# Kernel optimization log

Hardware: AMD Instinct MI355X
Metric: run time of the kernel (lower is better)

Reference implementation:

```python
import jax, jax.numpy as jnp
import numpy as np

B, S, D = 4, 2048, 1024
H, E = 16, 64  # n_heads, head_size; H*E == D


def setup_inputs() -> dict:
    key = jax.random.key(0)
    ks = jax.random.split(key, 6)
    sd = 1.0 / np.sqrt(D)
    x = jax.random.normal(ks[0], (B, S, D), dtype=jnp.float32)
    # per-head Q/K/V projection weights, stacked: [H, D, E]
    Wq = jax.random.uniform(ks[1], (H, D, E), jnp.float32, -sd, sd)
    Wk = jax.random.uniform(ks[2], (H, D, E), jnp.float32, -sd, sd)
    Wv = jax.random.uniform(ks[3], (H, D, E), jnp.float32, -sd, sd)
    Wp = jax.random.uniform(ks[4], (D, D), jnp.float32, -sd, sd)
    bp = jax.random.uniform(ks[5], (D,), jnp.float32, -sd, sd)
    return {"x": x, "Wq": Wq, "Wk": Wk, "Wv": Wv, "Wp": Wp, "bp": bp}


def reference(x, Wq, Wk, Wv, Wp, bp):
    # Per-head projections (all heads batched): [B, H, S, E]
    q = jnp.einsum('bsd,hde->bhse', x, Wq)
    k = jnp.einsum('bsd,hde->bhse', x, Wk)
    v = jnp.einsum('bsd,hde->bhse', x, Wv)
    scale = E ** -0.5
    # Full causal score matrix [B, H, S, S]
    wei = jnp.einsum('bhse,bhte->bhst', q, k) * scale
    causal = jnp.tril(jnp.ones((S, S), dtype=bool))
    wei = jnp.where(causal, wei, -jnp.inf)
    wei = jax.nn.softmax(wei, axis=-1)
    out = jnp.einsum('bhst,bhte->bhse', wei, v)
    # concat heads along feature dim: [B, S, H*E]
    out = out.transpose(0, 2, 1, 3).reshape(B, S, H * E)
    # output projection (dropout is identity in eval)
    return out @ Wp.T + bp
```

## Files before the change

kernel.cpp:

```cpp
#include <hip/hip_runtime.h>

#define B_ 4
#define S_ 2048
#define D_ 1024
#define H_ 16
#define E_ 64
#define M_ (B_*S_)

typedef __attribute__((ext_vector_type(8))) short short8;
typedef __attribute__((ext_vector_type(4))) float floatx4;

#define GLD16(g, l) __builtin_amdgcn_global_load_lds( \
    (const __attribute__((address_space(1))) unsigned*)(g), \
    (__attribute__((address_space(3))) unsigned*)(l), 16, 0, 0)

__device__ __forceinline__ ushort f2b(float f) {
    union { float f; unsigned u; } v; v.f = f;
    unsigned r = v.u + 0x7fffu + ((v.u >> 16) & 1u);
    return (ushort)(r >> 16);
}
__device__ __forceinline__ unsigned cvt_pk_bf16(float lo, float hi) {
    unsigned r;
    asm("v_cvt_pk_bf16_f32 %0, %1, %2" : "=v"(r) : "v"(lo), "v"(hi));
    return r;
}
__device__ __forceinline__ float fast_exp2(float x) {
#if __has_builtin(__builtin_amdgcn_exp2f)
    return __builtin_amdgcn_exp2f(x);
#else
    float r; asm("v_exp_f32 %0, %1" : "=v"(r) : "v"(x)); return r;
#endif
}
__device__ __forceinline__ float lane_pull(float v, int srclane) {
    return __int_as_float(__builtin_amdgcn_ds_bpermute(srclane << 2, __float_as_int(v)));
}

__global__ __launch_bounds__(256) void prologue(const float* __restrict__ x,
                                                const float* __restrict__ Wq,
                                                const float* __restrict__ Wk,
                                                const float* __restrict__ Wv,
                                                const float* __restrict__ Wp,
                                                ushort* __restrict__ xb,
                                                ushort* __restrict__ wpb,
                                                ushort* __restrict__ wt) {
    __shared__ __align__(16) ushort T[64 * 80];
    const int bid = blockIdx.x;
    const int t = threadIdx.x;

    if (bid < 2048) {
        const int n8 = (int)((size_t)M_ * D_ / 8);
        int i = bid * 256 + t;
        const int stride = 2048 * 256;
        for (; i < n8; i += stride) {
            float4 a = ((const float4*)x)[2 * i];
            float4 b = ((const float4*)x)[2 * i + 1];
            short8 o;
            o[0] = (short)f2b(a.x); o[1] = (short)f2b(a.y);
            o[2] = (short)f2b(a.z); o[3] = (short)f2b(a.w);
            o[4] = (short)f2b(b.x); o[5] = (short)f2b(b.y);
            o[6] = (short)f2b(b.z); o[7] = (short)f2b(b.w);
            ((short8*)xb)[i] = o;
        }
    } else if (bid < 2560) {
        int i = (bid - 2048) * 256 + t;
        float4 a = ((const float4*)Wp)[2 * i];
        float4 b = ((const float4*)Wp)[2 * i + 1];
        short8 o;
        o[0] = (short)f2b(a.x); o[1] = (short)f2b(a.y);
        o[2] = (short)f2b(a.z); o[3] = (short)f2b(a.w);
        o[4] = (short)f2b(b.x); o[5] = (short)f2b(b.y);
        o[6] = (short)f2b(b.z); o[7] = (short)f2b(b.w);
        ((short8*)wpb)[i] = o;
    } else {
        const int q = bid - 2560;
        const int g = q >> 4;
        const int d0 = (q & 15) * 64;
        const float* W = (g < 16 ? Wq : (g < 32 ? Wk : Wv)) + (size_t)(g & 15) * (D_ * E_);
        #pragma unroll
        for (int it = 0; it < 4; ++it) {
            int i = it * 256 + t;
            int r = i >> 4, c = i & 15;
            float4 xx = *(const float4*)(W + (size_t)(d0 + r) * E_ + c * 4);
            T[(c * 4 + 0) * 80 + r] = f2b(xx.x);
            T[(c * 4 + 1) * 80 + r] = f2b(xx.y);
            T[(c * 4 + 2) * 80 + r] = f2b(xx.z);
            T[(c * 4 + 3) * 80 + r] = f2b(xx.w);
        }
        __syncthreads();
        #pragma unroll
        for (int it = 0; it < 2; ++it) {
            int i = it * 256 + t;
            int e = i >> 3, c = i & 7;
            short8 xx = *(const short8*)&T[e * 80 + c * 8];
            *(short8*)&wt[((size_t)g * E_ + e) * D_ + d0 + c * 8] = xx;
        }
    }
}

__global__ __launch_bounds__(512) void gemm_qkv(const ushort* __restrict__ xb,
                                                const ushort* __restrict__ wt,
                                                ushort* __restrict__ qk,
                                                ushort* __restrict__ vt) {
    const int m0 = blockIdx.x * 256;
    const int n0 = blockIdx.y * 128;
    const int w  = n0 >> 10;

    __shared__ __align__(16) ushort As[2][256 * 32];
    __shared__ __align__(16) ushort Bs[2][128 * 32];

    const int t = threadIdx.x, l = t & 63, wid = t >> 6;
    const int wm = (wid & 3) * 64, wn = (wid >> 2) * 64;
    floatx4 acc[4][4] = {};

    {
        #pragma unroll
        for (int it = 0; it < 2; ++it) {
            int i = it * 512 + t;
            int r = i >> 2, cs = i & 3;
            int c = cs ^ ((r >> 1) & 3);
            GLD16(xb + (size_t)(m0 + r) * D_ + c * 8, &As[0][i * 8]);
        }
        int r = t >> 2, cs = t & 3;
        int c = cs ^ ((r >> 1) & 3);
        GLD16(wt + (size_t)(n0 + r) * D_ + c * 8, &Bs[0][t * 8]);
    }
    __syncthreads();

    int buf = 0;
    for (int k0 = 0; k0 < D_; k0 += 32) {
        if (k0 + 32 < D_) {
            #pragma unroll
            for (int it = 0; it < 2; ++it) {
                int i = it * 512 + t;
                int r = i >> 2, cs = i & 3;
                int c = cs ^ ((r >> 1) & 3);
                GLD16(xb + (size_t)(m0 + r) * D_ + k0 + 32 + c * 8, &As[buf ^ 1][i * 8]);
            }
            int r = t >> 2, cs = t & 3;
            int c = cs ^ ((r >> 1) & 3);
            GLD16(wt + (size_t)(n0 + r) * D_ + k0 + 32 + c * 8, &Bs[buf ^ 1][t * 8]);
        }

        short8 af[4], bf[4];
        #pragma unroll
        for (int mf = 0; mf < 4; ++mf) {
            int row = wm + 16 * mf + (l & 15);
            int c = (l >> 4) ^ ((row >> 1) & 3);
            af[mf] = *(const short8*)&As[buf][row * 32 + c * 8];
        }
        #pragma unroll
        for (int nf = 0; nf < 4; ++nf) {
            int row = wn + 16 * nf + (l & 15);
            int c = (l >> 4) ^ ((row >> 1) & 3);
            bf[nf] = *(const short8*)&Bs[buf][row * 32 + c * 8];
        }
        #pragma unroll
        for (int mf = 0; mf < 4; ++mf)
            #pragma unroll
            for (int nf = 0; nf < 4; ++nf)
                acc[mf][nf] = __builtin_amdgcn_mfma_f32_16x16x32_bf16(af[mf], bf[nf], acc[mf][nf], 0, 0, 0);

        __syncthreads();
        buf ^= 1;
    }

    if (w < 2) {
        ushort* outw = qk + (size_t)w * ((size_t)B_ * H_ * S_ * E_);
        #pragma unroll
        for (int mf = 0; mf < 4; ++mf)
            #pragma unroll
            for (int nf = 0; nf < 4; ++nf) {
                int n = n0 + wn + 16 * nf + (l & 15);
                int h = (n >> 6) & 15, e = n & 63;
                #pragma unroll
                for (int r = 0; r < 4; ++r) {
                    int m = m0 + wm + 16 * mf + (l >> 4) * 4 + r;
                    int b = m >> 11, s = m & (S_ - 1);
                    outw[((size_t)((b << 4) + h) * S_ + s) * E_ + e] = f2b(acc[mf][nf][r]);
                }
            }
    } else {
        #pragma unroll
        for (int mf = 0; mf < 4; ++mf) {
            int m = m0 + wm + 16 * mf + (l >> 4) * 4;
            int b = m >> 11, s = m & (S_ - 1);
            #pragma unroll
            for (int nf = 0; nf < 4; ++nf) {
                int n = n0 + wn + 16 * nf + (l & 15);
                int h = (n >> 6) & 15, e = n & 63;
                unsigned pk0 = cvt_pk_bf16(acc[mf][nf][0], acc[mf][nf][1]);
                unsigned pk1 = cvt_pk_bf16(acc[mf][nf][2], acc[mf][nf][3]);
                *(uint2*)&vt[((size_t)((b << 4) + h) * E_ + e) * S_ + s] = make_uint2(pk0, pk1);
            }
        }
    }
}

__global__ __launch_bounds__(256) void flash(const ushort* __restrict__ qg,
                                             const ushort* __restrict__ kg,
                                             const ushort* __restrict__ vtg,
                                             ushort* __restrict__ attn) {
    const int n = blockIdx.x;
    const int x = n >> 6;
    const int bh = n & 63;
    const int b = bh >> 4, h = bh & 15;
    const ushort* qb = qg + (size_t)bh * (S_ * E_);
    const ushort* kb = kg + (size_t)bh * (S_ * E_);
    const ushort* vb = vtg + (size_t)bh * (E_ * S_);

    __shared__ __align__(16) ushort QP[64 * 64];
    __shared__ __align__(16) ushort Ks[2][64 * 64];
    __shared__ __align__(16) ushort Vs[2][64 * 64];

    const int t = threadIdx.x, l = t & 63, wid = t >> 6;
    const float SC = 0.18033688f;
    const float NEG_INF = -__builtin_inff();
    const int g = l >> 4;
    const int qloc = l & 15;
    const int qts[2] = {x, 31 - x};
    ushort* Pw = &QP[wid * 1024];

    #pragma unroll 1
    for (int qi = 0; qi < 2; ++qi) {
        const int qt = qts[qi];

        #pragma unroll
        for (int it = 0; it < 2; ++it) {
            int i = it * 256 + t;
            int r = i >> 3, cs = i & 7, c = cs ^ (r & 7);
            GLD16(qb + (size_t)(qt * 64 + r) * E_ + c * 8, &QP[i * 8]);
            GLD16(kb + (size_t)r * E_ + c * 8, &Ks[0][i * 8]);
            GLD16(vb + (size_t)r * S_ + c * 8, &Vs[0][i * 8]);
        }
        __syncthreads();

        short8 qf[2];
        #pragma unroll
        for (int ks = 0; ks < 2; ++ks) {
            int row = wid * 16 + qloc;
            int c = (g + 4 * ks) ^ (row & 7);
            qf[ks] = *(const short8*)&QP[row * 64 + c * 8];
        }

        floatx4 o[4] = {};
        float mr = NEG_INF, lr = 0.f;

        int buf = 0;
        for (int jt = 0; jt <= qt; ++jt) {
            if (jt < qt) {
                #pragma unroll
                for (int it = 0; it < 2; ++it) {
                    int i = it * 256 + t;
                    int r = i >> 3, cs = i & 7, c = cs ^ (r & 7);
                    GLD16(kb + (size_t)((jt + 1) * 64 + r) * E_ + c * 8, &Ks[buf ^ 1][i * 8]);
                    GLD16(vb + (size_t)r * S_ + (jt + 1) * 64 + c * 8, &Vs[buf ^ 1][i * 8]);
                }
            }

            floatx4 s[4] = {};
            #pragma unroll
            for (int nf = 0; nf < 4; ++nf) {
                #pragma unroll
                for (int ks = 0; ks < 2; ++ks) {
                    int row = 16 * nf + qloc;
                    int c = (g + 4 * ks) ^ (row & 7);
                    short8 kf = *(const short8*)&Ks[buf][row * 64 + c * 8];
                    s[nf] = __builtin_amdgcn_mfma_f32_16x16x32_bf16(kf, qf[ks], s[nf], 0, 0, 0);
                }
            }

            if (jt == qt) {
                int qrow = wid * 16 + qloc;
                #pragma unroll
                for (int nf = 0; nf < 4; ++nf)
                    #pragma unroll
                    for (int r = 0; r < 4; ++r)
                        if (16 * nf + 4 * g + r > qrow) s[nf][r] = NEG_INF;
            }

            float mx = s[0][0];
            #pragma unroll
            for (int nf = 0; nf < 4; ++nf)
                #pragma unroll
                for (int r = 0; r < 4; ++r) mx = fmaxf(mx, s[nf][r]);
            mx = fmaxf(mx, __shfl_xor(mx, 16));
            mx = fmaxf(mx, __shfl_xor(mx, 32));
            bool ok = (mx - mr) * SC <= 8.0f;

            if (!__all(ok)) {
                float mn = fmaxf(mr, mx);
                float al = fast_exp2((mr - mn) * SC);
                mr = mn;
                lr *= al;
                #pragma unroll
                for (int r = 0; r < 4; ++r) {
                    float alq = lane_pull(al, 4 * g + r);
                    #pragma unroll
                    for (int nf = 0; nf < 4; ++nf) o[nf][r] *= alq;
                }
            }

            {
                float nm = -mr * SC;
                float rs = 0.f;
                #pragma unroll
                for (int nf = 0; nf < 4; ++nf)
                    #pragma unroll
                    for (int r = 0; r < 4; ++r) {
                        float p = fast_exp2(fmaf(s[nf][r], SC, nm));
                        s[nf][r] = p;
                        rs += p;
                    }
                lr += rs;
            }

            #pragma unroll
            for (int nf = 0; nf < 4; ++nf) {
                unsigned pk0 = cvt_pk_bf16(s[nf][0], s[nf][1]);
                unsigned pk1 = cvt_pk_bf16(s[nf][2], s[nf][3]);
                int chunk = 2 * nf + (g >> 1);
                int sw = chunk ^ (qloc & 7);
                int a = qloc * 64 + sw * 8 + 4 * (g & 1);
                *(uint2*)&Pw[a] = make_uint2(pk0, pk1);
            }

            short8 pf[2];
            #pragma unroll
            for (int ks = 0; ks < 2; ++ks) {
                int row = l & 15;
                int c = (g + 4 * ks) ^ (row & 7);
                pf[ks] = *(const short8*)&Pw[row * 64 + c * 8];
            }
            #pragma unroll
            for (int nf = 0; nf < 4; ++nf) {
                #pragma unroll
                for (int ks = 0; ks < 2; ++ks) {
                    int row = 16 * nf + (l & 15);
                    int c = (g + 4 * ks) ^ (row & 7);
                    short8 vf = *(const short8*)&Vs[buf][row * 64 + c * 8];
                    o[nf] = __builtin_amdgcn_mfma_f32_16x16x32_bf16(pf[ks], vf, o[nf], 0, 0, 0);
                }
            }

            __syncthreads();
            buf ^= 1;
        }

        lr += __shfl_xor(lr, 16);
        lr += __shfl_xor(lr, 32);
        float inv = 1.0f / lr;
        float il[4];
        #pragma unroll
        for (int r = 0; r < 4; ++r) il[r] = lane_pull(inv, 4 * g + r);

        #pragma unroll
        for (int nf = 0; nf < 4; ++nf) {
            int col = 16 * nf + qloc;
            #pragma unroll
            for (int rp = 0; rp < 2; ++rp) {
                unsigned pk = cvt_pk_bf16(o[nf][2 * rp] * il[2 * rp],
                                          o[nf][2 * rp + 1] * il[2 * rp + 1]);
                int row0 = g * 4 + 2 * rp;
                int a0 = row0 * 64 + (((col >> 3)) ^ (row0 & 7)) * 8 + (col & 7);
                int a1 = (row0 + 1) * 64 + (((col >> 3)) ^ ((row0 + 1) & 7)) * 8 + (col & 7);
                Pw[a0] = (ushort)pk;
                Pw[a1] = (ushort)(pk >> 16);
            }
        }
        #pragma unroll
        for (int it = 0; it < 2; ++it) {
            int i = it * 64 + l;
            int row = i >> 3, cc = i & 7;
            int c = cc ^ (row & 7);
            short8 vv = *(const short8*)&Pw[row * 64 + c * 8];
            int s_abs = qt * 64 + wid * 16 + row;
            *(short8*)&attn[((size_t)(b * S_ + s_abs)) * D_ + h * E_ + cc * 8] = vv;
        }
        __syncthreads();
    }
}

__global__ __launch_bounds__(256) void out_proj(const ushort* __restrict__ a,
                                                const ushort* __restrict__ wpb,
                                                const float* __restrict__ bp,
                                                float* __restrict__ out) {
    const int m0 = blockIdx.x * 128;
    const int n0 = blockIdx.y * 128;

    __shared__ __align__(16) ushort As[2][128 * 32];
    __shared__ __align__(16) ushort Bs[2][128 * 32];

    const int t = threadIdx.x, l = t & 63, wid = t >> 6;
    const int wm = (wid & 1) * 64, wn = (wid >> 1) * 64;
    floatx4 acc[4][4] = {};

    #pragma unroll
    for (int it = 0; it < 2; ++it) {
        int i = it * 256 + t;
        int r = i >> 2, cs = i & 3;
        int c = cs ^ ((r >> 1) & 3);
        GLD16(a + (size_t)(m0 + r) * D_ + c * 8, &As[0][i * 8]);
        GLD16(wpb + (size_t)(n0 + r) * D_ + c * 8, &Bs[0][i * 8]);
    }
    __syncthreads();

    int buf = 0;
    for (int k0 = 0; k0 < D_; k0 += 32) {
        if (k0 + 32 < D_) {
            #pragma unroll
            for (int it = 0; it < 2; ++it) {
                int i = it * 256 + t;
                int r = i >> 2, cs = i & 3;
                int c = cs ^ ((r >> 1) & 3);
                GLD16(a + (size_t)(m0 + r) * D_ + k0 + 32 + c * 8, &As[buf ^ 1][i * 8]);
                GLD16(wpb + (size_t)(n0 + r) * D_ + k0 + 32 + c * 8, &Bs[buf ^ 1][i * 8]);
            }
        }

        short8 af[4], bf[4];
        #pragma unroll
        for (int mf = 0; mf < 4; ++mf) {
            int row = wm + 16 * mf + (l & 15);
            int c = (l >> 4) ^ ((row >> 1) & 3);
            af[mf] = *(const short8*)&As[buf][row * 32 + c * 8];
        }
        #pragma unroll
        for (int nf = 0; nf < 4; ++nf) {
            int row = wn + 16 * nf + (l & 15);
            int c = (l >> 4) ^ ((row >> 1) & 3);
            bf[nf] = *(const short8*)&Bs[buf][row * 32 + c * 8];
        }
        #pragma unroll
        for (int mf = 0; mf < 4; ++mf)
            #pragma unroll
            for (int nf = 0; nf < 4; ++nf)
                acc[mf][nf] = __builtin_amdgcn_mfma_f32_16x16x32_bf16(af[mf], bf[nf], acc[mf][nf], 0, 0, 0);

        __syncthreads();
        buf ^= 1;
    }

    #pragma unroll
    for (int nf = 0; nf < 4; ++nf) {
        int col = n0 + wn + 16 * nf + (l & 15);
        float bias = bp[col];
        #pragma unroll
        for (int mf = 0; mf < 4; ++mf)
            #pragma unroll
            for (int r = 0; r < 4; ++r) {
                int m = m0 + wm + 16 * mf + (l >> 4) * 4 + r;
                out[(size_t)m * D_ + col] = acc[mf][nf][r] + bias;
            }
    }
}

extern "C" void kernel_launch(void* const* d_in, const int* in_sizes, int n_in,
                              void* d_out, int out_size, void* d_ws, size_t ws_size,
                              hipStream_t stream) {
    const float* x  = (const float*)d_in[0];
    const float* Wq = (const float*)d_in[1];
    const float* Wk = (const float*)d_in[2];
    const float* Wv = (const float*)d_in[3];
    const float* Wp = (const float*)d_in[4];
    const float* bp = (const float*)d_in[5];

    ushort* ws = (ushort*)d_ws;
    const size_t NX  = (size_t)M_ * D_;
    const size_t NW  = (size_t)48 * E_ * D_;
    const size_t NP  = (size_t)D_ * D_;
    const size_t QSZ = (size_t)B_ * H_ * S_ * E_;
    ushort* xb    = ws;
    ushort* wt    = xb + NX;
    ushort* wpb   = wt + NW;
    ushort* qk    = wpb + NP;
    ushort* vt    = qk + 2 * QSZ;
    ushort* attnb = vt + QSZ;

    prologue <<<3328, 256, 0, stream>>>(x, Wq, Wk, Wv, Wp, xb, wpb, wt);
    gemm_qkv <<<dim3(M_ / 256, 24), 512, 0, stream>>>(xb, wt, qk, vt);
    flash    <<<1024, 256, 0, stream>>>(qk, qk + QSZ, vt, attnb);
    out_proj <<<dim3(M_ / 128, D_ / 128), 256, 0, stream>>>(attnb, wpb, bp, (float*)d_out);
}
```

Before: 177.3 us.

## Switch flash attention to 32x32x16 MFMA with 2 waves per block

Rewrites the flash attention inner loop so each wave handles 32 query rows using 32x32x16 bf16 MFMAs instead of 16 rows with 16x16x32, and halves the block to 128 threads. The larger MFMA tiles are meant to cut LDS fragment reads per FLOP and drop one cross-lane shuffle step in the row max and sum reductions. In exchange each wave holds larger accumulators (more VGPRs), there are fewer waves per block to hide latency, and the epilogue writes scalar bf16 to LDS.

```diff
diff --git a/kernel.cpp b/kernel.cpp
--- a/kernel.cpp
+++ b/kernel.cpp
@@ -9,6 +9,7 @@
 
 typedef __attribute__((ext_vector_type(8))) short short8;
 typedef __attribute__((ext_vector_type(4))) float floatx4;
+typedef __attribute__((ext_vector_type(16))) float floatx16;
 
 #define GLD16(g, l) __builtin_amdgcn_global_load_lds( \
     (const __attribute__((address_space(1))) unsigned*)(g), \
@@ -196,7 +197,7 @@
     }
 }
 
-__global__ __launch_bounds__(256) void flash(const ushort* __restrict__ qg,
+__global__ __launch_bounds__(128) void flash(const ushort* __restrict__ qg,
                                              const ushort* __restrict__ kg,
                                              const ushort* __restrict__ vtg,
                                              ushort* __restrict__ attn) {
@@ -215,18 +216,18 @@
     const int t = threadIdx.x, l = t & 63, wid = t >> 6;
     const float SC = 0.18033688f;
     const float NEG_INF = -__builtin_inff();
-    const int g = l >> 4;
-    const int qloc = l & 15;
+    const int half = l >> 5;
+    const int lq = l & 31;
     const int qts[2] = {x, 31 - x};
-    ushort* Pw = &QP[wid * 1024];
+    ushort* Pw = &QP[wid * 2048];
 
     #pragma unroll 1
     for (int qi = 0; qi < 2; ++qi) {
         const int qt = qts[qi];
 
         #pragma unroll
-        for (int it = 0; it < 2; ++it) {
-            int i = it * 256 + t;
+        for (int it = 0; it < 4; ++it) {
+            int i = it * 128 + t;
             int r = i >> 3, cs = i & 7, c = cs ^ (r & 7);
             GLD16(qb + (size_t)(qt * 64 + r) * E_ + c * 8, &QP[i * 8]);
             GLD16(kb + (size_t)r * E_ + c * 8, &Ks[0][i * 8]);
@@ -234,56 +235,64 @@
         }
         __syncthreads();
 
-        short8 qf[2];
-        #pragma unroll
-        for (int ks = 0; ks < 2; ++ks) {
-            int row = wid * 16 + qloc;
-            int c = (g + 4 * ks) ^ (row & 7);
-            qf[ks] = *(const short8*)&QP[row * 64 + c * 8];
-        }
-
-        floatx4 o[4] = {};
+        short8 qf[4];
+        #pragma unroll
+        for (int ec = 0; ec < 4; ++ec) {
+            int row = wid * 32 + lq;
+            int cc = ec * 2 + half;
+            int c = cc ^ (row & 7);
+            qf[ec] = *(const short8*)&QP[row * 64 + c * 8];
+        }
+
+        floatx16 o[2] = {};
         float mr = NEG_INF, lr = 0.f;
 
         int buf = 0;
         for (int jt = 0; jt <= qt; ++jt) {
             if (jt < qt) {
                 #pragma unroll
-                for (int it = 0; it < 2; ++it) {
-                    int i = it * 256 + t;
+                for (int it = 0; it < 4; ++it) {
+                    int i = it * 128 + t;
                     int r = i >> 3, cs = i & 7, c = cs ^ (r & 7);
                     GLD16(kb + (size_t)((jt + 1) * 64 + r) * E_ + c * 8, &Ks[buf ^ 1][i * 8]);
                     GLD16(vb + (size_t)r * S_ + (jt + 1) * 64 + c * 8, &Vs[buf ^ 1][i * 8]);
                 }
             }
 
-            floatx4 s[4] = {};
-            #pragma unroll
-            for (int nf = 0; nf < 4; ++nf) {
-                #pragma unroll
-                for (int ks = 0; ks < 2; ++ks) {
-                    int row = 16 * nf + qloc;
-                    int c = (g + 4 * ks) ^ (row & 7);
+            floatx16 s[2] = {};
+            #pragma unroll
+            for (int ec = 0; ec < 4; ++ec) {
+                int cc = ec * 2 + half;
+                {
+                    int row = lq;
+                    int c = cc ^ (row & 7);
                     short8 kf = *(const short8*)&Ks[buf][row * 64 + c * 8];
-                    s[nf] = __builtin_amdgcn_mfma_f32_16x16x32_bf16(kf, qf[ks], s[nf], 0, 0, 0);
+                    s[0] = __builtin_amdgcn_mfma_f32_32x32x16_bf16(kf, qf[ec], s[0], 0, 0, 0);
+                }
+                {
+                    int row = 32 + lq;
+                    int c = cc ^ (row & 7);
+                    short8 kf = *(const short8*)&Ks[buf][row * 64 + c * 8];
+                    s[1] = __builtin_amdgcn_mfma_f32_32x32x16_bf16(kf, qf[ec], s[1], 0, 0, 0);
                 }
             }
 
             if (jt == qt) {
-                int qrow = wid * 16 + qloc;
-                #pragma unroll
-                for (int nf = 0; nf < 4; ++nf)
+                int qg_ = wid * 32 + lq;
+                #pragma unroll
+                for (int mt = 0; mt < 2; ++mt)
                     #pragma unroll
-                    for (int r = 0; r < 4; ++r)
-                        if (16 * nf + 4 * g + r > qrow) s[nf][r] = NEG_INF;
+                    for (int reg = 0; reg < 16; ++reg) {
+                        int kvloc = mt * 32 + (reg & 3) + 8 * (reg >> 2) + 4 * half;
+                        if (kvloc > qg_) s[mt][reg] = NEG_INF;
+                    }
             }
 
             float mx = s[0][0];
             #pragma unroll
-            for (int nf = 0; nf < 4; ++nf)
-                #pragma unroll
-                for (int r = 0; r < 4; ++r) mx = fmaxf(mx, s[nf][r]);
-            mx = fmaxf(mx, __shfl_xor(mx, 16));
+            for (int mt = 0; mt < 2; ++mt)
+                #pragma unroll
+                for (int reg = 0; reg < 16; ++reg) mx = fmaxf(mx, s[mt][reg]);
             mx = fmaxf(mx, __shfl_xor(mx, 32));
             bool ok = (mx - mr) * SC <= 8.0f;
 
@@ -293,10 +302,10 @@
                 mr = mn;
                 lr *= al;
                 #pragma unroll
-                for (int r = 0; r < 4; ++r) {
-                    float alq = lane_pull(al, 4 * g + r);
-                    #pragma unroll
-                    for (int nf = 0; nf < 4; ++nf) o[nf][r] *= alq;
+                for (int reg = 0; reg < 16; ++reg) {
+                    float alq = lane_pull(al, (reg & 3) + 8 * (reg >> 2) + 4 * half);
+                    o[0][reg] *= alq;
+                    o[1][reg] *= alq;
                 }
             }
 
@@ -304,77 +313,73 @@
                 float nm = -mr * SC;
                 float rs = 0.f;
                 #pragma unroll
-                for (int nf = 0; nf < 4; ++nf)
+                for (int mt = 0; mt < 2; ++mt)
                     #pragma unroll
-                    for (int r = 0; r < 4; ++r) {
-                        float p = fast_exp2(fmaf(s[nf][r], SC, nm));
-                        s[nf][r] = p;
+                    for (int reg = 0; reg < 16; ++reg) {
+                        float p = fast_exp2(fmaf(s[mt][reg], SC, nm));
+                        s[mt][reg] = p;
                         rs += p;
                     }
                 lr += rs;
             }
 
             #pragma unroll
-            for (int nf = 0; nf < 4; ++nf) {
-                unsigned pk0 = cvt_pk_bf16(s[nf][0], s[nf][1]);
-                unsigned pk1 = cvt_pk_bf16(s[nf][2], s[nf][3]);
-                int chunk = 2 * nf + (g >> 1);
-                int sw = chunk ^ (qloc & 7);
-                int a = qloc * 64 + sw * 8 + 4 * (g & 1);
-                *(uint2*)&Pw[a] = make_uint2(pk0, pk1);
-            }
-
-            short8 pf[2];
-            #pragma unroll
-            for (int ks = 0; ks < 2; ++ks) {
-                int row = l & 15;
-                int c = (g + 4 * ks) ^ (row & 7);
-                pf[ks] = *(const short8*)&Pw[row * 64 + c * 8];
-            }
-            #pragma unroll
-            for (int nf = 0; nf < 4; ++nf) {
-                #pragma unroll
-                for (int ks = 0; ks < 2; ++ks) {
-                    int row = 16 * nf + (l & 15);
-                    int c = (g + 4 * ks) ^ (row & 7);
+            for (int mt = 0; mt < 2; ++mt)
+                #pragma unroll
+                for (int r4 = 0; r4 < 4; ++r4) {
+                    unsigned pk0 = cvt_pk_bf16(s[mt][4 * r4 + 0], s[mt][4 * r4 + 1]);
+                    unsigned pk1 = cvt_pk_bf16(s[mt][4 * r4 + 2], s[mt][4 * r4 + 3]);
+                    int cc = mt * 4 + r4;
+                    int sc = cc ^ (lq & 7);
+                    *(uint2*)&Pw[lq * 64 + sc * 8 + 4 * half] = make_uint2(pk0, pk1);
+                }
+
+            short8 pf[4];
+            #pragma unroll
+            for (int kc = 0; kc < 4; ++kc) {
+                int cc = kc * 2 + half;
+                int c = cc ^ (lq & 7);
+                pf[kc] = *(const short8*)&Pw[lq * 64 + c * 8];
+            }
+            #pragma unroll
+            for (int nt = 0; nt < 2; ++nt)
+                #pragma unroll
+                for (int kc = 0; kc < 4; ++kc) {
+                    int row = nt * 32 + lq;
+                    int cc = kc * 2 + half;
+                    int c = cc ^ (row & 7);
                     short8 vf = *(const short8*)&Vs[buf][row * 64 + c * 8];
-                    o[nf] = __builtin_amdgcn_mfma_f32_16x16x32_bf16(pf[ks], vf, o[nf], 0, 0, 0);
-                }
-            }
+                    o[nt] = __builtin_amdgcn_mfma_f32_32x32x16_bf16(pf[kc], vf, o[nt], 0, 0, 0);
+                }
 
             __syncthreads();
             buf ^= 1;
         }
 
-        lr += __shfl_xor(lr, 16);
         lr += __shfl_xor(lr, 32);
         float inv = 1.0f / lr;
-        float il[4];
-        #pragma unroll
-        for (int r = 0; r < 4; ++r) il[r] = lane_pull(inv, 4 * g + r);
-
-        #pragma unroll
-        for (int nf = 0; nf < 4; ++nf) {
-            int col = 16 * nf + qloc;
-            #pragma unroll
-            for (int rp = 0; rp < 2; ++rp) {
-                unsigned pk = cvt_pk_bf16(o[nf][2 * rp] * il[2 * rp],
-                                          o[nf][2 * rp + 1] * il[2 * rp + 1]);
-                int row0 = g * 4 + 2 * rp;
-                int a0 = row0 * 64 + (((col >> 3)) ^ (row0 & 7)) * 8 + (col & 7);
-                int a1 = (row0 + 1) * 64 + (((col >> 3)) ^ ((row0 + 1) & 7)) * 8 + (col & 7);
-                Pw[a0] = (ushort)pk;
-                Pw[a1] = (ushort)(pk >> 16);
-            }
-        }
-        #pragma unroll
-        for (int it = 0; it < 2; ++it) {
+
+        #pragma unroll
+        for (int reg = 0; reg < 16; ++reg) {
+            int qrow = (reg & 3) + 8 * (reg >> 2) + 4 * half;
+            float il = lane_pull(inv, qrow);
+            #pragma unroll
+            for (int nt = 0; nt < 2; ++nt) {
+                unsigned pk = cvt_pk_bf16(o[nt][reg] * il, 0.f);
+                int e = nt * 32 + lq;
+                int cc = e >> 3;
+                int sc = cc ^ (qrow & 7);
+                Pw[qrow * 64 + sc * 8 + (e & 7)] = (ushort)pk;
+            }
+        }
+        #pragma unroll
+        for (int it = 0; it < 4; ++it) {
             int i = it * 64 + l;
-            int row = i >> 3, cc = i & 7;
-            int c = cc ^ (row & 7);
+            int row = i >> 3, ccx = i & 7;
+            int c = ccx ^ (row & 7);
             short8 vv = *(const short8*)&Pw[row * 64 + c * 8];
-            int s_abs = qt * 64 + wid * 16 + row;
-            *(short8*)&attn[((size_t)(b * S_ + s_abs)) * D_ + h * E_ + cc * 8] = vv;
+            int s_abs = qt * 64 + wid * 32 + row;
+            *(short8*)&attn[((size_t)(b * S_ + s_abs)) * D_ + h * E_ + ccx * 8] = vv;
         }
         __syncthreads();
     }
@@ -478,6 +483,6 @@
 
     prologue <<<3328, 256, 0, stream>>>(x, Wq, Wk, Wv, Wp, xb, wpb, wt);
     gemm_qkv <<<dim3(M_ / 256, 24), 512, 0, stream>>>(xb, wt, qk, vt);
-    flash    <<<1024, 256, 0, stream>>>(qk, qk + QSZ, vt, attnb);
+    flash    <<<1024, 128, 0, stream>>>(qk, qk + QSZ, vt, attnb);
     out_proj <<<dim3(M_ / 128, D_ / 128), 256, 0, stream>>>(attnb, wpb, bp, (float*)d_out);
 }
```

New measurement: 195.2 us. 1.1x slower.
